# Performance work log

Measured on AMD Instinct MI355X. Metric: run time of the kernel, lower is better.

## Reference

```python
import jax, jax.numpy as jnp
import numpy as np

B, D, K = 512, 128, 131072
TEMP = 0.07
PTR = 0  # queue_ptr starts at 0; B <= K so single contiguous write


def _normalize(x, axis):
    return x / jnp.linalg.norm(x, axis=axis, keepdims=True)


def setup_inputs() -> dict:
    key = jax.random.key(0)
    k = jax.random.split(key, 7)
    return {
        "predict0": jax.random.normal(k[0], (B, D), jnp.float32),
        "predict1": jax.random.normal(k[1], (B, D), jnp.float32),
        "project0": jax.random.normal(k[2], (B, D), jnp.float32),
        "project1": jax.random.normal(k[3], (B, D), jnp.float32),
        "queue": jax.random.normal(k[4], (D, K), jnp.float32),
        "queue_id": jax.random.randint(k[5], (K,), 0, 100000, jnp.int64) if jax.config.jax_enable_x64 else jax.random.randint(k[5], (K,), 0, 100000, jnp.int32),
        "ids": jax.random.randint(k[6], (B,), 0, 100000, jnp.int64) if jax.config.jax_enable_x64 else jax.random.randint(k[6], (B,), 0, 100000, jnp.int32),
    }


def _find_nn(proj, queue_n, queue_id, ids):
    # [B, K] similarity, mask out entries with same sample id, argmax, gather cols
    sim = proj @ queue_n                                   # [B, K]
    is_own = queue_id[None, :] == ids[:, None]             # [B, K]
    sim = jnp.where(is_own, jnp.float32(-1.0), sim)
    idx = jnp.argmax(sim, axis=1)                          # [B]
    return queue_n[:, idx]                                 # [D, B]


def _nnclr_loss(predicted, nn, temperature):
    # logits[i, j] = nn_i . predicted_j / T ; labels = arange(B)
    logits = (nn.T @ predicted.T) / temperature            # [B, B]
    logp = jax.nn.log_softmax(logits, axis=-1)
    return -jnp.mean(jnp.diagonal(logp))


def reference(predict0, predict1, project0, project1, queue, queue_id, ids):
    # forward_encoder's normalization (encoder itself is external and modeled out)
    p0 = _normalize(predict0, 1)
    p1 = _normalize(predict1, 1)
    z0 = _normalize(project0, 1)
    z1 = _normalize(project1, 1)
    queue_n = _normalize(queue, 0)  # queue stored normalized along dim 0

    # find_nn / queue are no_grad in the original
    nn0 = jax.lax.stop_gradient(_find_nn(jax.lax.stop_gradient(z0), queue_n, queue_id, ids))
    nn1 = jax.lax.stop_gradient(_find_nn(jax.lax.stop_gradient(z1), queue_n, queue_id, ids))

    loss0 = _nnclr_loss(p0, nn1, TEMP)
    loss1 = _nnclr_loss(p1, nn0, TEMP)
    loss = (loss0 + loss1) * 0.5

    # _dequeue_and_enqueue: ptr=0, B <= K -> contiguous slice write
    new_queue = jax.lax.dynamic_update_slice(queue_n, jax.lax.stop_gradient(z0.T), (0, PTR))
    new_queue_id = jax.lax.dynamic_update_slice(queue_id, ids, (PTR,))
    new_ptr = jnp.array((PTR + B) % K, dtype=queue_id.dtype)
    return loss, new_queue, new_queue_id, new_ptr
```

## Files before the change

kernel.cpp:

```cpp
#include <hip/hip_runtime.h>
#include <hip/hip_bf16.h>

typedef _Float16 half8 __attribute__((ext_vector_type(8)));
typedef _Float16 half4 __attribute__((ext_vector_type(4)));
typedef float f32x4 __attribute__((ext_vector_type(4)));

#define B 512
#define D 128
#define K 131072
#define TEMP 0.07f
#define NKB 512
#define KT_PER 16

#define INVN_OFF 0
#define Z0_OFF   131072
#define Z1_OFF   196608
#define P0_OFF   262144
#define P1_OFF   327680
#define ZF16_OFF 393216
#define QA_OFF   458752
#define PVAL_OFF 8847360
#define WKB_OFF  9371648
#define WVAL_OFF 9372672
#define IDX_OFF  9373696
#define LP_OFF   9374720

__global__ __launch_bounds__(128) void rownorm_k(
    const float* __restrict__ p0, const float* __restrict__ p1,
    const float* __restrict__ z0, const float* __restrict__ z1,
    float* __restrict__ w, _Float16* __restrict__ zf16) {
  int row = blockIdx.x & (B - 1);
  int which = blockIdx.x >> 9;
  const float* src; float* dst;
  switch (which) {
    case 0: src = z0; dst = w + Z0_OFF; break;
    case 1: src = z1; dst = w + Z1_OFF; break;
    case 2: src = p0; dst = w + P0_OFF; break;
    default: src = p1; dst = w + P1_OFF; break;
  }
  int tid = threadIdx.x;
  float v = src[row * D + tid];
  float s = v * v;
  #pragma unroll
  for (int o = 32; o; o >>= 1) s += __shfl_xor(s, o);
  __shared__ float sm[2];
  if ((tid & 63) == 0) sm[tid >> 6] = s;
  __syncthreads();
  float inv = rsqrtf(sm[0] + sm[1]);
  float nv = v * inv;
  dst[row * D + tid] = nv;
  if (which < 2) zf16[(which * B + row) * D + tid] = (_Float16)nv;
}

__global__ __launch_bounds__(256) void colq_k(
    const float* __restrict__ q, const int* __restrict__ qid,
    const int* __restrict__ ids, const float* __restrict__ w_z0,
    float* __restrict__ invn, float* __restrict__ out,
    _Float16* __restrict__ qA) {
  __shared__ float psum[8][128];
  __shared__ float invs[128];
  __shared__ _Float16 tile[128][136];
  int tid = threadIdx.x;
  int kb = blockIdx.x;
  int k0 = kb * 128;
  int kc = tid & 31, dg = tid >> 5;
  {
    float4 acc = {0.f, 0.f, 0.f, 0.f};
    for (int i = 0; i < 16; i++) {
      int d = dg * 16 + i;
      float4 v = *(const float4*)(q + (size_t)d * K + k0 + kc * 4);
      acc.x = fmaf(v.x, v.x, acc.x); acc.y = fmaf(v.y, v.y, acc.y);
      acc.z = fmaf(v.z, v.z, acc.z); acc.w = fmaf(v.w, v.w, acc.w);
    }
    *(float4*)&psum[dg][kc * 4] = acc;
  }
  __syncthreads();
  if (tid < 128) {
    float s = 0.f;
    #pragma unroll
    for (int g2 = 0; g2 < 8; g2++) s += psum[g2][tid];
    float inv = rsqrtf(s);
    invs[tid] = inv;
    invn[k0 + tid] = inv;
    int kk = k0 + tid;
    out[1 + (size_t)D * K + kk] = (float)((kk < B) ? ids[kk] : qid[kk]);
  }
  __syncthreads();
  {
    bool zblk = (k0 < B);
    float4 iv = *(const float4*)&invs[kc * 4];
    for (int i = 0; i < 16; i++) {
      int d = i * 8 + dg;
      float4 v = *(const float4*)(q + (size_t)d * K + k0 + kc * 4);
      float o0 = v.x * iv.x, o1 = v.y * iv.y, o2 = v.z * iv.z, o3 = v.w * iv.w;
      half4 t = {(_Float16)o0, (_Float16)o1, (_Float16)o2, (_Float16)o3};
      *(half4*)&tile[d][kc * 4] = t;
      float* oc = out + 1 + (size_t)d * K + k0 + kc * 4;
      if (zblk) {
        int col = k0 + kc * 4;
        oc[0] = w_z0[(size_t)(col + 0) * D + d];
        oc[1] = w_z0[(size_t)(col + 1) * D + d];
        oc[2] = w_z0[(size_t)(col + 2) * D + d];
        oc[3] = w_z0[(size_t)(col + 3) * D + d];
      } else {
        oc[0] = o0; oc[1] = o1; oc[2] = o2; oc[3] = o3;
      }
    }
  }
  __syncthreads();
  {
    int dc = tid >> 6, l = tid & 63;
    int g = l >> 4, c = l & 15;
    #pragma unroll
    for (int kt = 0; kt < 8; kt++) {
      half8 f;
      #pragma unroll
      for (int i = 0; i < 8; i++) {
        int d = g * 4 + (i & 3) + ((i >> 2) << 4) + dc * 32;
        f[i] = tile[d][kt * 16 + c];
      }
      int ktg = kb * 8 + kt;
      *(half8*)(qA + (size_t)((ktg * 4 + dc) * 64 + l) * 8) = f;
    }
  }
}

#define LOADAF(AF, Q4, KTG) do { \
  _Pragma("unroll") \
  for (int dc = 0; dc < 4; dc++) \
    AF[dc] = *(const half8*)(qA + (size_t)(((KTG) * 4 + dc) * 64 + lane) * 8); \
  Q4 = *(const int4*)(qid + (KTG) * 16 + g * 4); \
} while (0)

#define PROCESS(AF, Q4, KTG) do { \
  _Pragma("unroll") \
  for (int nt = 0; nt < 4; nt++) { \
    f32x4 acc = {0.f, 0.f, 0.f, 0.f}; \
    _Pragma("unroll") \
    for (int dc = 0; dc < 4; dc++) \
      acc = __builtin_amdgcn_mfma_f32_16x16x32_f16(AF[dc], bf[nt][dc], acc, 0, 0, 0); \
    _Pragma("unroll") \
    for (int r = 0; r < 4; r++) { \
      int qv_ = (r == 0) ? Q4.x : (r == 1) ? Q4.y : (r == 2) ? Q4.z : Q4.w; \
      float sm_ = (qv_ == myid[nt]) ? -1.0f : acc[r]; \
      best[nt] = fmaxf(best[nt], sm_); \
    } \
  } \
} while (0)

__global__ __launch_bounds__(256) void nnsearch_k(
    const _Float16* __restrict__ qA, const _Float16* __restrict__ zf16,
    const int* __restrict__ qid, const int* __restrict__ ids,
    float* __restrict__ pval) {
  int tid = threadIdx.x;
  int flat = blockIdx.x;
  int cls = flat & 7;
  int kb = cls * 64 + (flat >> 5);
  int rg = (flat >> 3) & 3;
  int wave = tid >> 6, lane = tid & 63;
  int g = lane >> 4, c = lane & 15;
  int rowbase = rg * 256 + wave * 64;

  half8 bf[4][4];
  int myid[4];
  #pragma unroll
  for (int nt = 0; nt < 4; nt++) {
    int row = rowbase + nt * 16 + c;
    myid[nt] = ids[row & (B - 1)];
    #pragma unroll
    for (int dc = 0; dc < 4; dc++) {
      const _Float16* zr = zf16 + row * D + dc * 32 + g * 4;
      half4 lo = *(const half4*)zr;
      half4 hi = *(const half4*)(zr + 16);
      half8 f = {lo[0], lo[1], lo[2], lo[3], hi[0], hi[1], hi[2], hi[3]};
      bf[nt][dc] = f;
    }
  }

  float best[4] = {-2.f, -2.f, -2.f, -2.f};
  int kt0 = kb * KT_PER;
  half8 afA[4], afB[4];
  int4 q4A, q4B;
  LOADAF(afA, q4A, kt0);
  for (int kt = 0; kt < KT_PER; kt += 2) {
    LOADAF(afB, q4B, kt0 + kt + 1);
    PROCESS(afA, q4A, kt0 + kt);
    if (kt + 2 < KT_PER) LOADAF(afA, q4A, kt0 + kt + 2);
    PROCESS(afB, q4B, kt0 + kt + 1);
  }

  #pragma unroll
  for (int nt = 0; nt < 4; nt++) {
    float v = best[nt];
    v = fmaxf(v, __shfl_xor(v, 16));
    v = fmaxf(v, __shfl_xor(v, 32));
    if (g == 0) {
      int row = rowbase + nt * 16 + c;
      pval[row * NKB + kb] = v;
    }
  }
}

__global__ __launch_bounds__(256) void nnreduce_k(
    const float* __restrict__ pval, int* __restrict__ wkb,
    float* __restrict__ wval) {
  int row = blockIdx.x;
  int tid = threadIdx.x;
  const float* p = pval + row * NKB;
  float a = p[tid], b = p[tid + 256];
  unsigned pa = (__float_as_uint(fmaf(a, 0.5f, 3.0f)) << 9) | (unsigned)(511 - tid);
  unsigned pb = (__float_as_uint(fmaf(b, 0.5f, 3.0f)) << 9) | (unsigned)(255 - tid);
  unsigned v = pa > pb ? pa : pb;
  #pragma unroll
  for (int o = 32; o; o >>= 1) {
    unsigned ov = __shfl_xor(v, o);
    v = v > ov ? v : ov;
  }
  __shared__ unsigned sv[4];
  if ((tid & 63) == 0) sv[tid >> 6] = v;
  __syncthreads();
  if (tid == 0) {
    #pragma unroll
    for (int wv = 1; wv < 4; wv++) v = v > sv[wv] ? v : sv[wv];
    int kb = 511 - (int)(v & 0x1FFu);
    wkb[row] = kb;
    wval[row] = pval[row * NKB + kb];
  }
}

__global__ __launch_bounds__(256) void nnfix_k(
    const _Float16* __restrict__ qA, const _Float16* __restrict__ zf16,
    const int* __restrict__ qid, const int* __restrict__ ids,
    const int* __restrict__ wkb, const float* __restrict__ wval,
    int* __restrict__ idxout) {
  int tid = threadIdx.x;
  int wave = tid >> 6, lane = tid & 63;
  int g = lane >> 4;
  int row = blockIdx.x * 4 + wave;
  int kb = wkb[row];
  float wv = wval[row];
  int myid = ids[row & (B - 1)];

  half8 bf[4];
  #pragma unroll
  for (int dc = 0; dc < 4; dc++) {
    const _Float16* zr = zf16 + row * D + dc * 32 + g * 4;
    half4 lo = *(const half4*)zr;
    half4 hi = *(const half4*)(zr + 16);
    half8 f = {lo[0], lo[1], lo[2], lo[3], hi[0], hi[1], hi[2], hi[3]};
    bf[dc] = f;
  }

  unsigned kbest = 0x7FFFFFFFu;
  int kt0 = kb * KT_PER;
  for (int kt = 0; kt < KT_PER; kt++) {
    int ktg = kt0 + kt;
    half8 af[4];
    #pragma unroll
    for (int dc = 0; dc < 4; dc++)
      af[dc] = *(const half8*)(qA + (size_t)((ktg * 4 + dc) * 64 + lane) * 8);
    int4 q4 = *(const int4*)(qid + ktg * 16 + g * 4);
    f32x4 acc = {0.f, 0.f, 0.f, 0.f};
    #pragma unroll
    for (int dc = 0; dc < 4; dc++)
      acc = __builtin_amdgcn_mfma_f32_16x16x32_f16(af[dc], bf[dc], acc, 0, 0, 0);
    #pragma unroll
    for (int r = 0; r < 4; r++) {
      int qv = (r == 0) ? q4.x : (r == 1) ? q4.y : (r == 2) ? q4.z : q4.w;
      float sm = (qv == myid) ? -1.0f : acc[r];
      if (sm == wv) {
        unsigned kk = (unsigned)(ktg * 16 + g * 4 + r);
        kbest = kbest < kk ? kbest : kk;
      }
    }
  }
  unsigned o1 = __shfl_xor(kbest, 16); kbest = kbest < o1 ? kbest : o1;
  unsigned o2 = __shfl_xor(kbest, 32); kbest = kbest < o2 ? kbest : o2;
  if (lane == 0) idxout[row] = (int)(kbest < (K - 1) ? kbest : (K - 1));
}

__global__ __launch_bounds__(256) void loss_k(
    const float* __restrict__ q, const float* __restrict__ invn,
    const int* __restrict__ idxout, const float* __restrict__ w,
    float* __restrict__ lpart) {
  int i0 = blockIdx.x * 8;
  int v = blockIdx.y;
  int tid = threadIdx.x;
  __shared__ float nns[8][D];
  __shared__ float rm[8][4], re[8][4], sdlds[8];
  #pragma unroll
  for (int ii = 0; ii < 4; ii++) {
    int i = ii * 2 + (tid >> 7);
    int d = tid & 127;
    int nnidx = idxout[(v ? 0 : B) + i0 + i];
    nns[i][d] = q[(size_t)d * K + nnidx] * invn[nnidx];
  }
  __syncthreads();
  const float* pr = w + (v ? P1_OFF : P0_OFF);
  const float* r0 = pr + tid * D;
  const float* r1 = pr + (tid + 256) * D;
  float a0[8] = {0, 0, 0, 0, 0, 0, 0, 0};
  float a1[8] = {0, 0, 0, 0, 0, 0, 0, 0};
  for (int d = 0; d < D; d += 4) {
    float4 x0 = *(const float4*)(r0 + d);
    float4 x1 = *(const float4*)(r1 + d);
    #pragma unroll
    for (int i = 0; i < 8; i++) {
      float4 n = *(const float4*)&nns[i][d];
      a0[i] = fmaf(x0.x, n.x, a0[i]); a0[i] = fmaf(x0.y, n.y, a0[i]);
      a0[i] = fmaf(x0.z, n.z, a0[i]); a0[i] = fmaf(x0.w, n.w, a0[i]);
      a1[i] = fmaf(x1.x, n.x, a1[i]); a1[i] = fmaf(x1.y, n.y, a1[i]);
      a1[i] = fmaf(x1.z, n.z, a1[i]); a1[i] = fmaf(x1.w, n.w, a1[i]);
    }
  }
  #pragma unroll
  for (int i = 0; i < 8; i++) {
    a0[i] *= (1.0f / TEMP);
    a1[i] *= (1.0f / TEMP);
  }
  #pragma unroll
  for (int i = 0; i < 8; i++) {
    int ig = i0 + i;
    if ((ig & 256) == 0) { if (tid == ig) sdlds[i] = a0[i]; }
    else { if (tid == (ig & 255)) sdlds[i] = a1[i]; }
  }
  int wv = tid >> 6;
  #pragma unroll
  for (int i = 0; i < 8; i++) {
    float m = fmaxf(a0[i], a1[i]);
    #pragma unroll
    for (int o = 32; o; o >>= 1) m = fmaxf(m, __shfl_xor(m, o));
    if ((tid & 63) == 0) rm[i][wv] = m;
  }
  __syncthreads();
  #pragma unroll
  for (int i = 0; i < 8; i++) {
    float m = fmaxf(fmaxf(rm[i][0], rm[i][1]), fmaxf(rm[i][2], rm[i][3]));
    float e = expf(a0[i] - m) + expf(a1[i] - m);
    #pragma unroll
    for (int o = 32; o; o >>= 1) e += __shfl_xor(e, o);
    if ((tid & 63) == 0) re[i][wv] = e;
  }
  __syncthreads();
  if (tid < 8) {
    int i = tid;
    float m = fmaxf(fmaxf(rm[i][0], rm[i][1]), fmaxf(rm[i][2], rm[i][3]));
    float s = re[i][0] + re[i][1] + re[i][2] + re[i][3];
    lpart[v * B + i0 + i] = sdlds[i] - m - logf(s);
  }
}

__global__ __launch_bounds__(256) void final_k(
    const float* __restrict__ lpart, float* __restrict__ out) {
  int tid = threadIdx.x;
  float s = lpart[tid] + lpart[tid + 256] + lpart[tid + 512] + lpart[tid + 768];
  #pragma unroll
  for (int o = 32; o; o >>= 1) s += __shfl_xor(s, o);
  __shared__ float sm[4];
  if ((tid & 63) == 0) sm[tid >> 6] = s;
  __syncthreads();
  if (tid == 0) {
    float total = sm[0] + sm[1] + sm[2] + sm[3];
    out[0] = -total * (1.0f / 1024.0f);
    out[1 + D * K + K] = 512.0f;
  }
}

extern "C" void kernel_launch(void* const* d_in, const int* in_sizes, int n_in,
                              void* d_out, int out_size, void* d_ws, size_t ws_size,
                              hipStream_t stream) {
  const float* p0 = (const float*)d_in[0];
  const float* p1 = (const float*)d_in[1];
  const float* z0 = (const float*)d_in[2];
  const float* z1 = (const float*)d_in[3];
  const float* q  = (const float*)d_in[4];
  const int* qid  = (const int*)d_in[5];
  const int* ids  = (const int*)d_in[6];
  float* out = (float*)d_out;
  float* w = (float*)d_ws;
  float* invn = w + INVN_OFF;
  _Float16* zf16 = (_Float16*)(w + ZF16_OFF);
  _Float16* qA   = (_Float16*)(w + QA_OFF);
  float* pval = w + PVAL_OFF;
  int* wkb    = (int*)(w + WKB_OFF);
  float* wval = w + WVAL_OFF;
  int* idxout = (int*)(w + IDX_OFF);
  float* lpart = w + LP_OFF;

  rownorm_k<<<2048, 128, 0, stream>>>(p0, p1, z0, z1, w, zf16);
  colq_k<<<K / 128, 256, 0, stream>>>(q, qid, ids, w + Z0_OFF, invn, out, qA);
  nnsearch_k<<<2048, 256, 0, stream>>>(qA, zf16, qid, ids, pval);
  nnreduce_k<<<1024, 256, 0, stream>>>(pval, wkb, wval);
  nnfix_k<<<256, 256, 0, stream>>>(qA, zf16, qid, ids, wkb, wval, idxout);
  dim3 gl(B / 8, 2);
  loss_k<<<gl, 256, 0, stream>>>(q, invn, idxout, w, lpart);
  final_k<<<1, 256, 0, stream>>>(lpart, out);
}
```

Measured before the change: 136.1 us.

## Stage queue tiles through LDS with async global_load_lds double buffering

The NN search kernel no longer has each of its four waves load the full A-fragment set for every k-tile straight from global memory. Each wave now loads one quarter of the tile into a shared double buffer using direct global-to-LDS loads, then all waves read the fragments from LDS. Queue ids are staged in LDS once per block. This is meant to cut redundant global traffic by a factor of four. In exchange it adds two workgroup barriers per k-tile plus manual waitcnt handling, which may serialize the waves.

After: 133.5 us. Within noise of the previous version (-1.9%).

```diff
diff --git a/kernel.cpp b/kernel.cpp
--- a/kernel.cpp
+++ b/kernel.cpp
@@ -24,6 +24,12 @@
 #define WVAL_OFF 9372672
 #define IDX_OFF  9373696
 #define LP_OFF   9374720
+
+__device__ __forceinline__ void gload_lds16(const _Float16* g, _Float16* l) {
+  __builtin_amdgcn_global_load_lds(
+      (const __attribute__((address_space(1))) unsigned int*)g,
+      (__attribute__((address_space(3))) unsigned int*)l, 16, 0, 0);
+}
 
 __global__ __launch_bounds__(128) void rownorm_k(
     const float* __restrict__ p0, const float* __restrict__ p1,
@@ -125,13 +131,6 @@
   }
 }
 
-#define LOADAF(AF, Q4, KTG) do { \
-  _Pragma("unroll") \
-  for (int dc = 0; dc < 4; dc++) \
-    AF[dc] = *(const half8*)(qA + (size_t)(((KTG) * 4 + dc) * 64 + lane) * 8); \
-  Q4 = *(const int4*)(qid + (KTG) * 16 + g * 4); \
-} while (0)
-
 #define PROCESS(AF, Q4, KTG) do { \
   _Pragma("unroll") \
   for (int nt = 0; nt < 4; nt++) { \
@@ -152,6 +151,8 @@
     const _Float16* __restrict__ qA, const _Float16* __restrict__ zf16,
     const int* __restrict__ qid, const int* __restrict__ ids,
     float* __restrict__ pval) {
+  __shared__ __align__(16) _Float16 qtile[2][2048];
+  __shared__ __align__(16) int qid_lds[256];
   int tid = threadIdx.x;
   int flat = blockIdx.x;
   int cls = flat & 7;
@@ -160,6 +161,13 @@
   int wave = tid >> 6, lane = tid & 63;
   int g = lane >> 4, c = lane & 15;
   int rowbase = rg * 256 + wave * 64;
+  int kt0 = kb * KT_PER;
+
+  gload_lds16(qA + (size_t)(((kt0 + 0) * 4 + wave) * 64 + lane) * 8,
+              &qtile[0][wave * 512]);
+  gload_lds16(qA + (size_t)(((kt0 + 1) * 4 + wave) * 64 + lane) * 8,
+              &qtile[1][wave * 512]);
+  qid_lds[tid] = qid[kb * 256 + tid];
 
   half8 bf[4][4];
   int myid[4];
@@ -176,17 +184,31 @@
       bf[nt][dc] = f;
     }
   }
+  __syncthreads();
 
   float best[4] = {-2.f, -2.f, -2.f, -2.f};
-  int kt0 = kb * KT_PER;
-  half8 afA[4], afB[4];
-  int4 q4A, q4B;
-  LOADAF(afA, q4A, kt0);
-  for (int kt = 0; kt < KT_PER; kt += 2) {
-    LOADAF(afB, q4B, kt0 + kt + 1);
-    PROCESS(afA, q4A, kt0 + kt);
-    if (kt + 2 < KT_PER) LOADAF(afA, q4A, kt0 + kt + 2);
-    PROCESS(afB, q4B, kt0 + kt + 1);
+  for (int kt = 0; kt < KT_PER; kt++) {
+    int cur = kt & 1;
+    half8 af[4];
+    #pragma unroll
+    for (int dc = 0; dc < 4; dc++)
+      af[dc] = *(const half8*)&qtile[cur][dc * 512 + lane * 8];
+    int4 q4 = *(const int4*)&qid_lds[kt * 16 + g * 4];
+    asm volatile("s_waitcnt lgkmcnt(0)" ::: "memory");
+    __builtin_amdgcn_sched_barrier(0);
+    __builtin_amdgcn_s_barrier();
+    __builtin_amdgcn_sched_barrier(0);
+    if (kt + 2 < KT_PER)
+      gload_lds16(qA + (size_t)(((kt0 + kt + 2) * 4 + wave) * 64 + lane) * 8,
+                  &qtile[cur][wave * 512]);
+    PROCESS(af, q4, kt0 + kt);
+    if (kt + 1 < KT_PER) {
+      if (kt + 2 < KT_PER) asm volatile("s_waitcnt vmcnt(1)" ::: "memory");
+      else                 asm volatile("s_waitcnt vmcnt(0)" ::: "memory");
+      __builtin_amdgcn_sched_barrier(0);
+      __builtin_amdgcn_s_barrier();
+      __builtin_amdgcn_sched_barrier(0);
+    }
   }
 
   #pragma unroll
```
